# Kernel tuning notes

Measured on AMD Instinct MI355X. Metric: run time of the kernel, lower is better.

Reference implementation:

```python
import jax, jax.numpy as jnp
import numpy as np

BATCH = 32
DIM = 768


def _packed_pool_indices(seq_lens_np, kernel_size, stride):
    """Host-side (static) index construction for packed ragged avg-pool.

    Returns gather indices [total_y, K] into the packed x and a validity mask,
    mirroring the Triton forward_pooling_kernel's masked window loads.
    """
    sl = np.asarray(seq_lens_np, np.int64)
    x_cu = np.concatenate([np.zeros(1, np.int64), np.cumsum(sl)])
    # compute_output_shape: ceil_div(max(0, L - K), S) + 1, 0 if L == 0
    y_lens = np.where(sl == 0, 0, -(-np.maximum(sl - kernel_size, 0) // stride) + 1)
    y_cu = np.concatenate([np.zeros(1, np.int64), np.cumsum(y_lens)])
    total_y = int(y_cu[-1])
    b = np.repeat(np.arange(len(sl)), y_lens)                 # batch id per output token
    j = np.arange(total_y) - np.repeat(y_cu[:-1], y_lens)    # local output position
    pos = j[:, None] * stride + np.arange(kernel_size)[None, :]  # [total_y, K] input pos
    lens_b = sl[b][:, None]
    valid = pos < lens_b                                       # mask = idx_x_seq < x_seq_len
    idx = x_cu[b][:, None] + np.minimum(pos, np.maximum(lens_b - 1, 0))
    return jnp.asarray(idx, jnp.int32), jnp.asarray(valid)


def setup_inputs() -> dict:
    key = jax.random.key(0)
    seq_lens = (1024 + 97 * np.arange(BATCH)).astype(np.int32)  # ragged, total = 80880
    total_tokens = int(seq_lens.sum())
    x = jax.random.normal(key, (total_tokens, DIM), dtype=jnp.float32)
    return {"x": x, "seq_lens": jnp.asarray(seq_lens), "kernel_size": 2, "stride": 2}


def reference(x, seq_lens, kernel_size, stride):
    # seq_lens are structural constants (define the ragged layout)
    idx, valid = _packed_pool_indices(np.asarray(jax.device_get(seq_lens)), kernel_size, stride)
    gathered = x[idx]                            # [total_y, K, D]
    m = valid.astype(x.dtype)[:, :, None]        # [total_y, K, 1]
    # masked average over the kernel window: norm = 1 / count of valid taps
    return (gathered * m).sum(axis=1) / m.sum(axis=1)
```

## Files before the change

### kernel.cpp

```cpp
#include <hip/hip_runtime.h>


#define DIM   768
#define D4    (DIM / 4)
#define MAXB  128

__global__ __launch_bounds__(256) void packed_avgpool_kernel(
    const float4* __restrict__ x,
    const int*    __restrict__ seq_lens,
    const int*    __restrict__ kptr,
    const int*    __restrict__ sptr,
    float4*       __restrict__ out,
    int batch, long long n4)
{
    __shared__ int s_xcu[MAXB + 1];
    __shared__ int s_ycu[MAXB + 1];
    __shared__ int s_len[MAXB];

    const int K = kptr[0];
    const int S = sptr[0];

    if (threadIdx.x == 0) {
        int xc = 0, yc = 0;
        s_xcu[0] = 0;
        s_ycu[0] = 0;
        for (int i = 0; i < batch; ++i) {
            int L = seq_lens[i];
            s_len[i] = L;
            xc += L;
            int over = (L > K) ? (L - K) : 0;
            int yl = (L == 0) ? 0 : (over + S - 1) / S + 1;
            yc += yl;
            s_xcu[i + 1] = xc;
            s_ycu[i + 1] = yc;
        }
    }
    __syncthreads();

    const long long gstride = (long long)gridDim.x * blockDim.x;
    for (long long e = (long long)blockIdx.x * blockDim.x + threadIdx.x;
         e < n4; e += gstride) {
        int row = (int)(e / D4);
        int col = (int)(e - (long long)row * D4);

        int lo = 0, hi = batch - 1;
        while (lo < hi) {
            int mid = (lo + hi + 1) >> 1;
            if (s_ycu[mid] <= row) lo = mid; else hi = mid - 1;
        }
        const int b = lo;
        const int j = row - s_ycu[b];
        const int L = s_len[b];
        const long long base = (long long)s_xcu[b];

        float4 acc = make_float4(0.f, 0.f, 0.f, 0.f);
        int cnt = 0;
        const int p0 = j * S;
        #pragma unroll 4
        for (int k = 0; k < K; ++k) {
            int pos = p0 + k;
            if (pos < L) {
                float4 v = x[(base + pos) * D4 + col];
                acc.x += v.x; acc.y += v.y; acc.z += v.z; acc.w += v.w;
                ++cnt;
            }
        }
        const float inv = 1.0f / (float)cnt;
        acc.x *= inv; acc.y *= inv; acc.z *= inv; acc.w *= inv;
        out[e] = acc;
    }
}

extern "C" void kernel_launch(void* const* d_in, const int* in_sizes, int n_in,
                              void* d_out, int out_size, void* d_ws, size_t ws_size,
                              hipStream_t stream) {
    const float* x        = (const float*)d_in[0];
    const int*   seq_lens = (const int*)d_in[1];
    const int*   kptr     = (const int*)d_in[2];
    const int*   sptr     = (const int*)d_in[3];
    float*       out      = (float*)d_out;

    const int batch = in_sizes[1];
    const long long n4 = (long long)out_size / 4;

    int blocks = 4096;
    long long need = (n4 + 255) / 256;
    if (need < blocks) blocks = (int)(need > 0 ? need : 1);

    packed_avgpool_kernel<<<blocks, 256, 0, stream>>>(
        (const float4*)x, seq_lens, kptr, sptr, (float4*)out, batch, n4);
}
```

Measured before the change: 374.2 us.

## Map one block per output row with wave-scan batch lookup

```diff
diff --git a/kernel.cpp b/kernel.cpp
--- a/kernel.cpp
+++ b/kernel.cpp
@@ -1,92 +1,90 @@
 #include <hip/hip_runtime.h>
 
 
-#define DIM   768
-#define D4    (DIM / 4)
-#define MAXB  128
+#define DIM 768
+#define D4  (DIM / 4)
 
-__global__ __launch_bounds__(256) void packed_avgpool_kernel(
+typedef float vfloat4 __attribute__((ext_vector_type(4)));
+
+__global__ __launch_bounds__(D4) void packed_avgpool_rows(
     const float4* __restrict__ x,
     const int*    __restrict__ seq_lens,
     const int*    __restrict__ kptr,
     const int*    __restrict__ sptr,
     float4*       __restrict__ out,
-    int batch, long long n4)
+    int batch)
 {
-    __shared__ int s_xcu[MAXB + 1];
-    __shared__ int s_ycu[MAXB + 1];
-    __shared__ int s_len[MAXB];
+    __shared__ int s_base;
+    __shared__ int s_p0;
+    __shared__ int s_L;
+    __shared__ int s_K;
 
-    const int K = kptr[0];
-    const int S = sptr[0];
+    const int row = blockIdx.x;
 
-    if (threadIdx.x == 0) {
-        int xc = 0, yc = 0;
-        s_xcu[0] = 0;
-        s_ycu[0] = 0;
-        for (int i = 0; i < batch; ++i) {
-            int L = seq_lens[i];
-            s_len[i] = L;
-            xc += L;
-            int over = (L > K) ? (L - K) : 0;
-            int yl = (L == 0) ? 0 : (over + S - 1) / S + 1;
-            yc += yl;
-            s_xcu[i + 1] = xc;
-            s_ycu[i + 1] = yc;
+    if (threadIdx.x < 64) {
+        const int lane = threadIdx.x;
+        const int K = kptr[0];
+        const int S = sptr[0];
+        int L = (lane < batch) ? seq_lens[lane] : 0;
+        int over = (L > K) ? (L - K) : 0;
+        int yl   = (L == 0) ? 0 : (over + S - 1) / S + 1;
+
+        int xs = L, ys = yl;
+        #pragma unroll
+        for (int off = 1; off < 64; off <<= 1) {
+            int xv = __shfl_up(xs, off);
+            int yv = __shfl_up(ys, off);
+            if (lane >= off) { xs += xv; ys += yv; }
+        }
+
+        unsigned long long bal = __ballot(ys <= row);
+        int b   = (int)__popcll(bal);
+        int xcu = (b == 0) ? 0 : __shfl(xs, b - 1);
+        int ycu = (b == 0) ? 0 : __shfl(ys, b - 1);
+        int Lb  = __shfl(L, b);
+        if (lane == 0) {
+            s_base = xcu;
+            s_p0   = (row - ycu) * S;
+            s_L    = Lb;
+            s_K    = K;
         }
     }
     __syncthreads();
 
-    const long long gstride = (long long)gridDim.x * blockDim.x;
-    for (long long e = (long long)blockIdx.x * blockDim.x + threadIdx.x;
-         e < n4; e += gstride) {
-        int row = (int)(e / D4);
-        int col = (int)(e - (long long)row * D4);
+    const int K    = s_K;
+    const int L    = s_L;
+    const int p0   = s_p0;
+    const int base = s_base;
+    const int col  = threadIdx.x;
 
-        int lo = 0, hi = batch - 1;
-        while (lo < hi) {
-            int mid = (lo + hi + 1) >> 1;
-            if (s_ycu[mid] <= row) lo = mid; else hi = mid - 1;
-        }
-        const int b = lo;
-        const int j = row - s_ycu[b];
-        const int L = s_len[b];
-        const long long base = (long long)s_xcu[b];
-
-        float4 acc = make_float4(0.f, 0.f, 0.f, 0.f);
-        int cnt = 0;
-        const int p0 = j * S;
-        #pragma unroll 4
-        for (int k = 0; k < K; ++k) {
-            int pos = p0 + k;
-            if (pos < L) {
-                float4 v = x[(base + pos) * D4 + col];
-                acc.x += v.x; acc.y += v.y; acc.z += v.z; acc.w += v.w;
-                ++cnt;
-            }
-        }
-        const float inv = 1.0f / (float)cnt;
-        acc.x *= inv; acc.y *= inv; acc.z *= inv; acc.w *= inv;
-        out[e] = acc;
+    float4 acc = make_float4(0.f, 0.f, 0.f, 0.f);
+    float  cnt = 0.f;
+    for (int k = 0; k < K; ++k) {
+        int   pos  = p0 + k;
+        int   cpos = (pos < L) ? pos : (L - 1);
+        float m    = (pos < L) ? 1.f : 0.f;
+        float4 v = x[(long long)(base + cpos) * D4 + col];
+        acc.x += m * v.x; acc.y += m * v.y; acc.z += m * v.z; acc.w += m * v.w;
+        cnt   += m;
     }
+    const float inv = 1.0f / cnt;
+    vfloat4 r = { acc.x * inv, acc.y * inv, acc.z * inv, acc.w * inv };
+    __builtin_nontemporal_store(
+        r, (vfloat4*)&out[(long long)row * D4 + col]);
 }
 
 extern "C" void kernel_launch(void* const* d_in, const int* in_sizes, int n_in,
                               void* d_out, int out_size, void* d_ws, size_t ws_size,
                               hipStream_t stream) {
-    const float* x        = (const float*)d_in[0];
-    const int*   seq_lens = (const int*)d_in[1];
-    const int*   kptr     = (const int*)d_in[2];
-    const int*   sptr     = (const int*)d_in[3];
-    float*       out      = (float*)d_out;
+    const float4* x        = (const float4*)d_in[0];
+    const int*    seq_lens = (const int*)d_in[1];
+    const int*    kptr     = (const int*)d_in[2];
+    const int*    sptr     = (const int*)d_in[3];
+    float4*       out      = (float4*)d_out;
 
-    const int batch = in_sizes[1];
-    const long long n4 = (long long)out_size / 4;
+    const int batch   = in_sizes[1];
+    const int total_y = out_size / DIM;
 
-    int blocks = 4096;
-    long long need = (n4 + 255) / 256;
-    if (need < blocks) blocks = (int)(need > 0 ? need : 1);
-
-    packed_avgpool_kernel<<<blocks, 256, 0, stream>>>(
-        (const float4*)x, seq_lens, kptr, sptr, (float4*)out, batch, n4);
+    packed_avgpool_rows<<<total_y, D4, 0, stream>>>(
+        x, seq_lens, kptr, sptr, out, batch);
 }
```

New measurement: 372.4 us. No clear change (-0.5%).
